# Performance work log

Measured on AMD Instinct MI355X. Metric: run time of the kernel, lower is better.

## Reference

```python
import jax, jax.numpy as jnp
import numpy as np

N_HEAD = 16
W = 128  # one-sided window = attention_window // 2


def setup_inputs() -> dict:
    key = jax.random.key(0)
    ks = jax.random.split(key, 6)
    B, S, D = 4, 1536, 1024
    init = lambda k: jax.random.normal(k, (D, D), jnp.float32) * 0.02
    return {
        "x": jax.random.normal(ks[0], (B, S, D), jnp.float32),
        "Wq": init(ks[1]), "bq": jnp.zeros((D,), jnp.float32),
        "Wk": init(ks[2]),
        "Wv": init(ks[3]), "bv": jnp.zeros((D,), jnp.float32),
        "Wo": init(ks[4]), "bo": jnp.zeros((D,), jnp.float32),
    }


def _local_attention(q, k, v, w):
    """Sliding-window attention. q,k,v: [B,H,S,Dh]; q,k pre-scaled.
    Returns context [B,H,S,Dh] and banded logits qk [B,S,H,2w+1] (fp32)."""
    B, H, S, Dh = q.shape
    C = S // w  # number of w-sized query chunks
    pad = [(0, 0), (0, 0), (w, w), (0, 0)]
    kp = jnp.pad(k, pad)
    vp = jnp.pad(v, pad)
    # key/value chunks: chunk c sees padded positions [c*w, c*w + 3w)
    idx = jnp.arange(C)[:, None] * w + jnp.arange(3 * w)[None, :]  # [C,3w]
    kc = kp[:, :, idx]                      # [B,H,C,3w,Dh]
    vc = vp[:, :, idx]                      # [B,H,C,3w,Dh]
    qc = q.reshape(B, H, C, w, Dh)          # [B,H,C,w,Dh]
    scores = jnp.einsum('bhcxd,bhcyd->bhcxy', qc, kc)  # [B,H,C,w,3w]
    # extract diagonal band: query x attends to chunk-local keys y = x .. x+2w
    xi = jnp.arange(w)[:, None]             # [w,1]
    jj = jnp.arange(2 * w + 1)[None, :]     # [1,2w+1]
    y = xi + jj                             # [w,2w+1], values in [0,3w)
    band = jnp.take_along_axis(scores, y[None, None, None], axis=-1)  # [B,H,C,w,2w+1]
    # mask positions whose absolute key index falls outside [0,S)
    key_pos = jnp.arange(C)[:, None, None] * w + xi[None] + jj[None] - w  # [C,w,2w+1]
    valid = (key_pos >= 0) & (key_pos < S)
    band = jnp.where(valid[None, None], band, -jnp.inf)
    prob = jax.nn.softmax(band.astype(jnp.float32), axis=-1).astype(q.dtype)
    # scatter band probs back to chunk layout, then contract with value chunks
    scat = jnp.zeros_like(scores).at[..., xi, y].set(prob)  # [B,H,C,w,3w]
    ctx = jnp.einsum('bhcxy,bhcyd->bhcxd', scat, vc).reshape(B, H, S, Dh)
    qk = band.astype(jnp.float32).reshape(B, H, S, 2 * w + 1).transpose(0, 2, 1, 3)
    return ctx, qk


def reference(x, Wq, bq, Wk, Wv, bv, Wo, bo):
    B, S, D = x.shape
    H, Dh = N_HEAD, D // N_HEAD
    scale = Dh ** (-0.25)
    q = ((x @ Wq.T + bq).reshape(B, S, H, Dh).transpose(0, 2, 1, 3)) * scale
    k = ((x @ Wk.T).reshape(B, S, H, Dh).transpose(0, 2, 1, 3)) * scale
    v = (x @ Wv.T + bv).reshape(B, S, H, Dh).transpose(0, 2, 1, 3)
    ctx, qk = _local_attention(q, k, v, W)
    wv = ctx.transpose(0, 2, 1, 3).reshape(B, S, D)
    out = wv @ Wo.T + bo
    return out, qk
```

## Files before the change

kernel.cpp:

```cpp
#include <hip/hip_runtime.h>

#define S_LEN  1536
#define NH     16
#define DHEAD  64
#define WIN    128
#define BAND   257
#define DMODEL 1024
#define BATCH  4
#define MROWS  (BATCH * S_LEN)

#define SQ    32
#define SWIN  (SQ + 2*WIN)
#define WKEYS 320
#define PST   296

#define NEG_BIG (-3.0e38f)

typedef __attribute__((ext_vector_type(8))) short frag_ab;
typedef __attribute__((ext_vector_type(4))) float frag_cd;
typedef __attribute__((ext_vector_type(8))) unsigned short ushort8v;

__device__ __forceinline__ unsigned short f2bf(float f) {
  unsigned u = __float_as_uint(f);
  u += 0x7FFFu + ((u >> 16) & 1u);
  return (unsigned short)(u >> 16);
}
__device__ __forceinline__ float bf2f(unsigned short h) {
  return __uint_as_float(((unsigned)h) << 16);
}

__device__ __forceinline__ void gload16(const unsigned short* g, unsigned short* l) {
  __builtin_amdgcn_global_load_lds(
      (const __attribute__((address_space(1))) unsigned int*)g,
      (__attribute__((address_space(3))) unsigned int*)l, 16, 0, 0);
}

__global__ __launch_bounds__(256)
void convert_hilo(const float* __restrict__ src, unsigned short* __restrict__ hi,
                  unsigned short* __restrict__ lo, int n4)
{
  const int i = blockIdx.x * 256 + threadIdx.x;
  if (i >= n4) return;
  const float4 v = reinterpret_cast<const float4*>(src)[i];
  unsigned short h0 = f2bf(v.x), h1 = f2bf(v.y), h2 = f2bf(v.z), h3 = f2bf(v.w);
  unsigned short l0 = f2bf(v.x - bf2f(h0)), l1 = f2bf(v.y - bf2f(h1));
  unsigned short l2 = f2bf(v.z - bf2f(h2)), l3 = f2bf(v.w - bf2f(h3));
  uint2 hp, lp;
  hp.x = (unsigned)h0 | ((unsigned)h1 << 16); hp.y = (unsigned)h2 | ((unsigned)h3 << 16);
  lp.x = (unsigned)l0 | ((unsigned)l1 << 16); lp.y = (unsigned)l2 | ((unsigned)l3 << 16);
  reinterpret_cast<uint2*>(hi)[i] = hp;
  reinterpret_cast<uint2*>(lo)[i] = lp;
}

__global__ __launch_bounds__(256)
void copy_f4(const float4* __restrict__ src, float4* __restrict__ dst, int n4)
{
  const int i = blockIdx.x * 256 + threadIdx.x;
  if (i < n4) dst[i] = src[i];
}

__global__ __launch_bounds__(256)
void mfma_gemm_bt(const unsigned short* __restrict__ Ah_g,
                  const unsigned short* __restrict__ Al_g,
                  const unsigned short* __restrict__ Bh_g,
                  const unsigned short* __restrict__ Bl_g,
                  const float* __restrict__ bias, float scale,
                  float* __restrict__ Cf,
                  unsigned short* __restrict__ Ch,
                  unsigned short* __restrict__ Cl, int mode)
{
  __shared__ __align__(16) unsigned short Ah[128*32];
  __shared__ __align__(16) unsigned short Al[128*32];
  __shared__ __align__(16) unsigned short Bh[64*32];
  __shared__ __align__(16) unsigned short Bl[64*32];

  const int t    = threadIdx.x;
  const int wave = t >> 6, lane = t & 63;
  const int wr   = wave >> 1, wc = wave & 1;
  const int m0   = blockIdx.y * 128;
  const int n0   = blockIdx.x * 64;

  frag_cd acc[4][2];
#pragma unroll
  for (int i = 0; i < 4; ++i)
#pragma unroll
    for (int j = 0; j < 2; ++j) acc[i][j] = (frag_cd){0.f,0.f,0.f,0.f};

  const int srow = lane >> 2;
  const int scol = (lane & 3) * 8;
  const unsigned short* pa0 = Ah_g + (size_t)(m0 + wave*32      + srow) * DMODEL + scol;
  const unsigned short* pa1 = Ah_g + (size_t)(m0 + wave*32 + 16 + srow) * DMODEL + scol;
  const unsigned short* qa0 = Al_g + (size_t)(m0 + wave*32      + srow) * DMODEL + scol;
  const unsigned short* qa1 = Al_g + (size_t)(m0 + wave*32 + 16 + srow) * DMODEL + scol;
  const unsigned short* pb  = Bh_g + (size_t)(n0 + wave*16      + srow) * DMODEL + scol;
  const unsigned short* qb  = Bl_g + (size_t)(n0 + wave*16      + srow) * DMODEL + scol;
  unsigned short* lA0 = &Ah[(wave*32)*32];
  unsigned short* lA1 = &Ah[(wave*32+16)*32];
  unsigned short* lL0 = &Al[(wave*32)*32];
  unsigned short* lL1 = &Al[(wave*32+16)*32];
  unsigned short* lB  = &Bh[(wave*16)*32];
  unsigned short* lBl = &Bl[(wave*16)*32];

  const int l16  = lane & 15;
  const int koff = (lane >> 4) * 8;
  int ofsA[4], ofsB[2];
#pragma unroll
  for (int i = 0; i < 4; ++i) ofsA[i] = (wr*64 + i*16 + l16)*32 + koff;
#pragma unroll
  for (int j = 0; j < 2; ++j) ofsB[j] = (wc*32 + j*16 + l16)*32 + koff;

  for (int k0 = 0; k0 < DMODEL; k0 += 32) {
    gload16(pa0, lA0); gload16(pa1, lA1);
    gload16(qa0, lL0); gload16(qa1, lL1);
    gload16(pb,  lB);  gload16(qb,  lBl);
    pa0 += 32; pa1 += 32; qa0 += 32; qa1 += 32; pb += 32; qb += 32;
    __syncthreads();

    frag_ab ah[4], alr[4], bh[2], blr[2];
#pragma unroll
    for (int i = 0; i < 4; ++i) {
      ah[i]  = *reinterpret_cast<const frag_ab*>(&Ah[ofsA[i]]);
      alr[i] = *reinterpret_cast<const frag_ab*>(&Al[ofsA[i]]);
    }
#pragma unroll
    for (int j = 0; j < 2; ++j) {
      bh[j]  = *reinterpret_cast<const frag_ab*>(&Bh[ofsB[j]]);
      blr[j] = *reinterpret_cast<const frag_ab*>(&Bl[ofsB[j]]);
    }
#pragma unroll
    for (int i = 0; i < 4; ++i)
#pragma unroll
      for (int j = 0; j < 2; ++j) {
        acc[i][j] = __builtin_amdgcn_mfma_f32_16x16x32_bf16(ah[i],  bh[j],  acc[i][j], 0,0,0);
        acc[i][j] = __builtin_amdgcn_mfma_f32_16x16x32_bf16(ah[i],  blr[j], acc[i][j], 0,0,0);
        acc[i][j] = __builtin_amdgcn_mfma_f32_16x16x32_bf16(alr[i], bh[j],  acc[i][j], 0,0,0);
      }
    __syncthreads();
  }

  const int rg = lane >> 4;
#pragma unroll
  for (int j = 0; j < 2; ++j) {
    const int n = n0 + wc*32 + j*16 + l16;
    const float bval = bias ? bias[n] : 0.f;
#pragma unroll
    for (int i = 0; i < 4; ++i) {
#pragma unroll
      for (int r = 0; r < 4; ++r) {
        const int m = m0 + wr*64 + i*16 + rg*4 + r;
        const float v = (acc[i][j][r] + bval) * scale;
        if (mode) {
          const int b = m / S_LEN;
          const int s = m - b * S_LEN;
          const int hh = n >> 6, dh = n & 63;
          const size_t idx = ((size_t)((b*NH + hh)*S_LEN + s))*DHEAD + dh;
          const unsigned short hv = f2bf(v);
          Ch[idx] = hv;
          Cl[idx] = f2bf(v - bf2f(hv));
        } else {
          Cf[(size_t)m * DMODEL + n] = v;
        }
      }
    }
  }
}

__global__ __launch_bounds__(256)
void attn_fused(const unsigned short* __restrict__ Qh_g, const unsigned short* __restrict__ Ql_g,
                const unsigned short* __restrict__ Kh_g, const unsigned short* __restrict__ Kl_g,
                const unsigned short* __restrict__ Vh_g, const unsigned short* __restrict__ Vl_g,
                float* __restrict__ qk,
                unsigned short* __restrict__ ctx_hi, unsigned short* __restrict__ ctx_lo)
{
  __shared__ __align__(16) unsigned char arena[59904];
  unsigned short* Khs = (unsigned short*)(arena);
  unsigned short* Kls = (unsigned short*)(arena + 20480);
  unsigned short* Qhs = (unsigned short*)(arena + 40960);
  unsigned short* Qls = (unsigned short*)(arena + 43008);
  unsigned short* Pth = (unsigned short*)(arena);
  unsigned short* Ptl = (unsigned short*)(arena + 18944);
  float*          red = (float*)(arena + 37888);
  unsigned short* Vth = (unsigned short*)(arena + 40960);
  unsigned short* Vtl = (unsigned short*)(arena + 50432);

  const int t    = threadIdx.x;
  const int wave = t >> 6, lane = t & 63;

  const int lid  = blockIdx.x;
  const int xcd  = lid & 7;
  const int idx  = lid >> 3;
  const int qblk = xcd*6 + (idx % 6);
  const int hb   = idx / 6;
  const int h    = hb & 15, b = hb >> 4;
  const int qa0  = qblk * SQ;
  const int ws0  = qa0 - WIN;

  const size_t ho = (size_t)(b*NH + h) * S_LEN * DHEAD;
  const unsigned short* Qh = Qh_g + ho;
  const unsigned short* Ql = Ql_g + ho;
  const unsigned short* Kh = Kh_g + ho;
  const unsigned short* Kl = Kl_g + ho;
  const unsigned short* Vh = Vh_g + ho;
  const unsigned short* Vl = Vl_g + ho;

  const int l16  = lane & 15;
  const int grp  = lane >> 4;
  const int koff = grp * 8;
  const int srow = lane >> 2;
  const int scol = (lane & 3) * 8;

  frag_cd acc[2][5];
#pragma unroll
  for (int tm = 0; tm < 2; ++tm)
#pragma unroll
    for (int tn = 0; tn < 5; ++tn) acc[tm][tn] = (frag_cd){0.f,0.f,0.f,0.f};

  for (int p = 0; p < 2; ++p) {
    const int d0 = p * 32;
    if (p) __syncthreads();
#pragma unroll
    for (int i = 0; i < 5; ++i) {
      const int r0 = wave*80 + i*16;
      const ptrdiff_t g = (ptrdiff_t)(ws0 + r0 + srow) * DHEAD + d0 + scol;
      gload16(Kh + g, &Khs[r0*32]);
      gload16(Kl + g, &Kls[r0*32]);
    }
    if (wave < 2) {
      const unsigned short* src = wave ? Ql : Qh;
      unsigned short* dst = wave ? Qls : Qhs;
#pragma unroll
      for (int i = 0; i < 2; ++i) {
        const ptrdiff_t g = (ptrdiff_t)(qa0 + i*16 + srow) * DHEAD + d0 + scol;
        gload16(src + g, &dst[i*16*32]);
      }
    }
    __syncthreads();

    frag_ab ah[2], al[2];
#pragma unroll
    for (int tm = 0; tm < 2; ++tm) {
      const int o = (tm*16 + l16)*32 + koff;
      ah[tm] = *reinterpret_cast<const frag_ab*>(&Qhs[o]);
      al[tm] = *reinterpret_cast<const frag_ab*>(&Qls[o]);
    }
#pragma unroll
    for (int tn = 0; tn < 5; ++tn) {
      const int o = (wave*80 + tn*16 + l16)*32 + koff;
      frag_ab bh = *reinterpret_cast<const frag_ab*>(&Khs[o]);
      frag_ab bl = *reinterpret_cast<const frag_ab*>(&Kls[o]);
#pragma unroll
      for (int tm = 0; tm < 2; ++tm) {
        acc[tm][tn] = __builtin_amdgcn_mfma_f32_16x16x32_bf16(ah[tm], bh, acc[tm][tn], 0,0,0);
        acc[tm][tn] = __builtin_amdgcn_mfma_f32_16x16x32_bf16(ah[tm], bl, acc[tm][tn], 0,0,0);
        acc[tm][tn] = __builtin_amdgcn_mfma_f32_16x16x32_bf16(al[tm], bh, acc[tm][tn], 0,0,0);
      }
    }
  }

#pragma unroll
  for (int tm = 0; tm < 2; ++tm)
#pragma unroll
    for (int tn = 0; tn < 5; ++tn)
#pragma unroll
      for (int r = 0; r < 4; ++r) {
        const int x  = tm*16 + grp*4 + r;
        const int yw = wave*80 + tn*16 + l16;
        const int j  = yw - x;
        const int kp = ws0 + yw;
        const bool ok = (j >= 0) & (j < BAND) & (kp >= 0) & (kp < S_LEN);
        acc[tm][tn][r] = ok ? acc[tm][tn][r] : NEG_BIG;
      }
#pragma unroll
  for (int tm = 0; tm < 2; ++tm)
#pragma unroll
    for (int r = 0; r < 4; ++r) {
      const int x = tm*16 + grp*4 + r;
      float* qrow = qk + ((size_t)(b*S_LEN + qa0 + x)*NH + h) * BAND;
#pragma unroll
      for (int tn = 0; tn < 5; ++tn) {
        const int yw = wave*80 + tn*16 + l16;
        const int j  = yw - x;
        if (j >= 0 && j < BAND) qrow[j] = acc[tm][tn][r];
      }
    }

  __syncthreads();

  ushort8v vreg[5];
  const unsigned short* vsrc = (wave & 2) ? Vl : Vh;
  unsigned short*       vdst = (wave & 2) ? Vtl : Vth;
  const int dsub = (wave & 1) * 8;

  auto loadV = [&](int c) {
    const int d0 = c*16 + dsub;
#pragma unroll
    for (int it = 0; it < 5; ++it) {
      const int y = it*64 + lane;
      ushort8v v = {0,0,0,0,0,0,0,0};
      if (y < SWIN) {
        const int kp = ws0 + y;
        if (kp >= 0 && kp < S_LEN)
          v = *reinterpret_cast<const ushort8v*>(vsrc + (size_t)kp*DHEAD + d0);
      }
      vreg[it] = v;
    }
  };
  auto writeV = [&]() {
#pragma unroll
    for (int it = 0; it < 5; ++it) {
      const int y = it*64 + lane;
      if (y < SWIN) {
#pragma unroll
        for (int e = 0; e < 8; ++e) vdst[(dsub+e)*PST + y] = vreg[it][e];
      }
    }
  };

  loadV(0);
  float gm[2][4];
#pragma unroll
  for (int tm = 0; tm < 2; ++tm)
#pragma unroll
    for (int r = 0; r < 4; ++r) {
      float m = acc[tm][0][r];
#pragma unroll
      for (int tn = 1; tn < 5; ++tn) m = fmaxf(m, acc[tm][tn][r]);
      m = fmaxf(m, __shfl_xor(m, 1, 64));
      m = fmaxf(m, __shfl_xor(m, 2, 64));
      m = fmaxf(m, __shfl_xor(m, 4, 64));
      m = fmaxf(m, __shfl_xor(m, 8, 64));
      gm[tm][r] = m;
      if (l16 == 0) red[(0*4 + wave)*32 + tm*16 + grp*4 + r] = m;
    }
  {
    const uint4 z = make_uint4(0u,0u,0u,0u);
    uint4* pz = reinterpret_cast<uint4*>(arena);
    for (int i = t; i < 37888/16; i += 256) pz[i] = z;
  }
  writeV();
  loadV(1);
  __syncthreads();

#pragma unroll
  for (int tm = 0; tm < 2; ++tm)
#pragma unroll
    for (int r = 0; r < 4; ++r) {
      const int x = tm*16 + grp*4 + r;
      float m = red[0*128 + 0*32 + x];
      m = fmaxf(m, red[0*128 + 1*32 + x]);
      m = fmaxf(m, red[0*128 + 2*32 + x]);
      m = fmaxf(m, red[0*128 + 3*32 + x]);
      gm[tm][r] = m;
      float s = 0.f;
#pragma unroll
      for (int tn = 0; tn < 5; ++tn) {
        const float e = __expf(acc[tm][tn][r] - m);
        acc[tm][tn][r] = e;
        s += e;
      }
      s += __shfl_xor(s, 1, 64);
      s += __shfl_xor(s, 2, 64);
      s += __shfl_xor(s, 4, 64);
      s += __shfl_xor(s, 8, 64);
      if (l16 == 0) red[(1*4 + wave)*32 + x] = s;
    }
  __syncthreads();

#pragma unroll
  for (int tm = 0; tm < 2; ++tm)
#pragma unroll
    for (int r = 0; r < 4; ++r) {
      const int x = tm*16 + grp*4 + r;
      const float gs = red[128 + 0*32 + x] + red[128 + 1*32 + x]
                     + red[128 + 2*32 + x] + red[128 + 3*32 + x];
      const float inv = 1.f / gs;
#pragma unroll
      for (int tn = 0; tn < 5; ++tn) {
        const int yw = wave*80 + tn*16 + l16;
        const int j  = yw - x;
        if (yw < SWIN && j >= 0 && j < BAND) {
          const float p = acc[tm][tn][r] * inv;
          const unsigned short ph = f2bf(p);
          Pth[x*PST + yw] = ph;
          Ptl[x*PST + yw] = f2bf(p - bf2f(ph));
        }
      }
    }
  __syncthreads();

  for (int c = 0; c < 4; ++c) {
    if ((wave & 1) == 0) {
      const int wr = wave >> 1;
      frag_cd a = (frag_cd){0.f,0.f,0.f,0.f};
#pragma unroll
      for (int ks = 0; ks < SWIN/32; ++ks) {
        const int kk = ks*32 + koff;
        frag_ab ph = *reinterpret_cast<const frag_ab*>(&Pth[(wr*16 + l16)*PST + kk]);
        frag_ab pl = *reinterpret_cast<const frag_ab*>(&Ptl[(wr*16 + l16)*PST + kk]);
        frag_ab vh = *reinterpret_cast<const frag_ab*>(&Vth[l16*PST + kk]);
        frag_ab vl = *reinterpret_cast<const frag_ab*>(&Vtl[l16*PST + kk]);
        a = __builtin_amdgcn_mfma_f32_16x16x32_bf16(ph, vh, a, 0,0,0);
        a = __builtin_amdgcn_mfma_f32_16x16x32_bf16(ph, vl, a, 0,0,0);
        a = __builtin_amdgcn_mfma_f32_16x16x32_bf16(pl, vh, a, 0,0,0);
      }
      const int d = c*16 + l16;
#pragma unroll
      for (int r = 0; r < 4; ++r) {
        const int x = wr*16 + grp*4 + r;
        const size_t oidx = ((size_t)(b*S_LEN + qa0 + x))*DMODEL + h*DHEAD + d;
        const float v = a[r];
        const unsigned short hv = f2bf(v);
        ctx_hi[oidx] = hv;
        ctx_lo[oidx] = f2bf(v - bf2f(hv));
      }
    }
    __syncthreads();
    if (c < 3) {
      writeV();
      if (c < 2) loadV(c + 2);
      __syncthreads();
    }
  }
}

extern "C" void kernel_launch(void* const* d_in, const int* in_sizes, int n_in,
                              void* d_out, int out_size, void* d_ws, size_t ws_size,
                              hipStream_t stream) {
  const float* x  = (const float*)d_in[0];
  const float* Wq = (const float*)d_in[1];
  const float* bq = (const float*)d_in[2];
  const float* Wk = (const float*)d_in[3];
  const float* Wv = (const float*)d_in[4];
  const float* bv = (const float*)d_in[5];
  const float* Wo = (const float*)d_in[6];
  const float* bo = (const float*)d_in[7];

  float* out = (float*)d_out;
  float* qk  = out + (size_t)MROWS * DMODEL;

  const size_t NX = (size_t)MROWS * DMODEL;
  const size_t NW = (size_t)DMODEL * DMODEL;

  unsigned short* xh  = (unsigned short*)qk;
  unsigned short* xl  = xh  + NX;
  unsigned short* wqh = xl  + NX;
  unsigned short* wql = wqh + NW;
  unsigned short* wkh = wql + NW;
  unsigned short* wkl = wkh + NW;
  unsigned short* wvh = wkl + NW;
  unsigned short* wvl = wvh + NW;

  unsigned short* Qh = (unsigned short*)d_ws;
  unsigned short* Ql = Qh + NX;
  unsigned short* Kh = Ql + NX;
  unsigned short* Kl = Kh + NX;
  unsigned short* Vh = Kl + NX;
  unsigned short* Vl = Vh + NX;

  unsigned short* ctxh = (unsigned short*)out;
  unsigned short* ctxl = ctxh + NX;
  unsigned short* woh  = Kh;
  unsigned short* wol  = Kh + NW;
  float* outTmp = (float*)d_ws;

  const float scale = 0.35355339059327373f;

  dim3 blk(256);
  hipLaunchKernelGGL(convert_hilo, dim3(NX/1024), blk, 0, stream, x,  xh,  xl,  (int)(NX/4));
  hipLaunchKernelGGL(convert_hilo, dim3(NW/1024), blk, 0, stream, Wq, wqh, wql, (int)(NW/4));
  hipLaunchKernelGGL(convert_hilo, dim3(NW/1024), blk, 0, stream, Wk, wkh, wkl, (int)(NW/4));
  hipLaunchKernelGGL(convert_hilo, dim3(NW/1024), blk, 0, stream, Wv, wvh, wvl, (int)(NW/4));

  dim3 gg(DMODEL/64, MROWS/128);
  hipLaunchKernelGGL(mfma_gemm_bt, gg, blk, 0, stream, xh, xl, wqh, wql, bq,      scale,
                     (float*)nullptr, Qh, Ql, 1);
  hipLaunchKernelGGL(mfma_gemm_bt, gg, blk, 0, stream, xh, xl, wkh, wkl, nullptr, scale,
                     (float*)nullptr, Kh, Kl, 1);
  hipLaunchKernelGGL(mfma_gemm_bt, gg, blk, 0, stream, xh, xl, wvh, wvl, bv,      1.0f,
                     (float*)nullptr, Vh, Vl, 1);

  hipLaunchKernelGGL(attn_fused, dim3((S_LEN/SQ)*NH*BATCH), blk, 0, stream,
                     Qh, Ql, Kh, Kl, Vh, Vl, qk, ctxh, ctxl);

  hipLaunchKernelGGL(convert_hilo, dim3(NW/1024), blk, 0, stream, Wo, woh, wol, (int)(NW/4));

  hipLaunchKernelGGL(mfma_gemm_bt, gg, blk, 0, stream, ctxh, ctxl, woh, wol, bo, 1.0f,
                     outTmp, (unsigned short*)nullptr, (unsigned short*)nullptr, 0);
  hipLaunchKernelGGL(copy_f4, dim3(NX/1024), blk, 0, stream,
                     (const float4*)outTmp, (float4*)out, (int)(NX/4));
}
```

Measured before the change: 509.7 us.

## Split PV stage into producer/consumer waves and shrink LDS for higher occupancy

The P·V stage is reorganised so each 16-wide B tile packs the high and low halves of V for eight head dims. This needs two MFMAs per k-step instead of three, and a lane shuffle folds the two halves back together. Waves 2-3 become V loaders with RA/RB register double-buffering, while waves 0-1 do the MFMAs with the P-high fragments held in registers across chunks. The single V buffer cuts shared memory and the launch bounds now request 3 blocks per CU, aiming for more concurrency. In exchange, half the waves sit out the matrix work, the stage runs eight synchronised chunks instead of four, and the extra P-low×V-low product is harmless but wasted work.

```diff
diff --git a/kernel.cpp b/kernel.cpp
--- a/kernel.cpp
+++ b/kernel.cpp
@@ -165,14 +165,14 @@
   }
 }
 
-__global__ __launch_bounds__(256)
+__global__ __launch_bounds__(256, 3)
 void attn_fused(const unsigned short* __restrict__ Qh_g, const unsigned short* __restrict__ Ql_g,
                 const unsigned short* __restrict__ Kh_g, const unsigned short* __restrict__ Kl_g,
                 const unsigned short* __restrict__ Vh_g, const unsigned short* __restrict__ Vl_g,
                 float* __restrict__ qk,
                 unsigned short* __restrict__ ctx_hi, unsigned short* __restrict__ ctx_lo)
 {
-  __shared__ __align__(16) unsigned char arena[59904];
+  __shared__ __align__(16) unsigned char arena[48384];
   unsigned short* Khs = (unsigned short*)(arena);
   unsigned short* Kls = (unsigned short*)(arena + 20480);
   unsigned short* Qhs = (unsigned short*)(arena + 40960);
@@ -180,8 +180,7 @@
   unsigned short* Pth = (unsigned short*)(arena);
   unsigned short* Ptl = (unsigned short*)(arena + 18944);
   float*          red = (float*)(arena + 37888);
-  unsigned short* Vth = (unsigned short*)(arena + 40960);
-  unsigned short* Vtl = (unsigned short*)(arena + 50432);
+  unsigned short* Vs  = (unsigned short*)(arena + 38912);
 
   const int t    = threadIdx.x;
   const int wave = t >> 6, lane = t & 63;
@@ -286,13 +285,12 @@
 
   __syncthreads();
 
-  ushort8v vreg[5];
-  const unsigned short* vsrc = (wave & 2) ? Vl : Vh;
-  unsigned short*       vdst = (wave & 2) ? Vtl : Vth;
-  const int dsub = (wave & 1) * 8;
-
-  auto loadV = [&](int c) {
-    const int d0 = c*16 + dsub;
+  const unsigned short* vsrc = (wave == 3) ? Vl : Vh;
+  const int vrow0 = (wave == 3) ? 8 : 0;
+  ushort8v RA[5], RB[5];
+
+  auto loadVto = [&](int c, ushort8v* R) {
+    const int d0 = c*8;
 #pragma unroll
     for (int it = 0; it < 5; ++it) {
       const int y = it*64 + lane;
@@ -302,22 +300,21 @@
         if (kp >= 0 && kp < S_LEN)
           v = *reinterpret_cast<const ushort8v*>(vsrc + (size_t)kp*DHEAD + d0);
       }
-      vreg[it] = v;
+      R[it] = v;
     }
   };
-  auto writeV = [&]() {
+  auto writeVfrom = [&](ushort8v* R) {
 #pragma unroll
     for (int it = 0; it < 5; ++it) {
       const int y = it*64 + lane;
       if (y < SWIN) {
 #pragma unroll
-        for (int e = 0; e < 8; ++e) vdst[(dsub+e)*PST + y] = vreg[it][e];
+        for (int e = 0; e < 8; ++e) Vs[(vrow0 + e)*PST + y] = R[it][e];
       }
     }
   };
 
-  loadV(0);
-  float gm[2][4];
+  if (wave >= 2) loadVto(0, RA);
 #pragma unroll
   for (int tm = 0; tm < 2; ++tm)
 #pragma unroll
@@ -329,7 +326,6 @@
       m = fmaxf(m, __shfl_xor(m, 2, 64));
       m = fmaxf(m, __shfl_xor(m, 4, 64));
       m = fmaxf(m, __shfl_xor(m, 8, 64));
-      gm[tm][r] = m;
       if (l16 == 0) red[(0*4 + wave)*32 + tm*16 + grp*4 + r] = m;
     }
   {
@@ -337,10 +333,10 @@
     uint4* pz = reinterpret_cast<uint4*>(arena);
     for (int i = t; i < 37888/16; i += 256) pz[i] = z;
   }
-  writeV();
-  loadV(1);
+  if (wave >= 2) writeVfrom(RA);
   __syncthreads();
 
+  if (wave >= 2) loadVto(1, RA);
 #pragma unroll
   for (int tm = 0; tm < 2; ++tm)
 #pragma unroll
@@ -350,7 +346,6 @@
       m = fmaxf(m, red[0*128 + 1*32 + x]);
       m = fmaxf(m, red[0*128 + 2*32 + x]);
       m = fmaxf(m, red[0*128 + 3*32 + x]);
-      gm[tm][r] = m;
       float s = 0.f;
 #pragma unroll
       for (int tn = 0; tn < 5; ++tn) {
@@ -388,38 +383,48 @@
     }
   __syncthreads();
 
-  for (int c = 0; c < 4; ++c) {
-    if ((wave & 1) == 0) {
-      const int wr = wave >> 1;
-      frag_cd a = (frag_cd){0.f,0.f,0.f,0.f};
-#pragma unroll
-      for (int ks = 0; ks < SWIN/32; ++ks) {
+  frag_ab phf[9];
+  if (wave < 2) {
+#pragma unroll
+    for (int ks = 0; ks < 9; ++ks)
+      phf[ks] = *reinterpret_cast<const frag_ab*>(&Pth[(wave*16 + l16)*PST + ks*32 + koff]);
+  }
+
+#pragma unroll
+  for (int c = 0; c < 8; ++c) {
+    frag_cd pacc = (frag_cd){0.f,0.f,0.f,0.f};
+    if (wave < 2) {
+#pragma unroll
+      for (int ks = 0; ks < 9; ++ks) {
         const int kk = ks*32 + koff;
-        frag_ab ph = *reinterpret_cast<const frag_ab*>(&Pth[(wr*16 + l16)*PST + kk]);
-        frag_ab pl = *reinterpret_cast<const frag_ab*>(&Ptl[(wr*16 + l16)*PST + kk]);
-        frag_ab vh = *reinterpret_cast<const frag_ab*>(&Vth[l16*PST + kk]);
-        frag_ab vl = *reinterpret_cast<const frag_ab*>(&Vtl[l16*PST + kk]);
-        a = __builtin_amdgcn_mfma_f32_16x16x32_bf16(ph, vh, a, 0,0,0);
-        a = __builtin_amdgcn_mfma_f32_16x16x32_bf16(ph, vl, a, 0,0,0);
-        a = __builtin_amdgcn_mfma_f32_16x16x32_bf16(pl, vh, a, 0,0,0);
-      }
-      const int d = c*16 + l16;
-#pragma unroll
-      for (int r = 0; r < 4; ++r) {
-        const int x = wr*16 + grp*4 + r;
-        const size_t oidx = ((size_t)(b*S_LEN + qa0 + x))*DMODEL + h*DHEAD + d;
-        const float v = a[r];
-        const unsigned short hv = f2bf(v);
-        ctx_hi[oidx] = hv;
-        ctx_lo[oidx] = f2bf(v - bf2f(hv));
-      }
+        frag_ab pl = *reinterpret_cast<const frag_ab*>(&Ptl[(wave*16 + l16)*PST + kk]);
+        frag_ab vb = *reinterpret_cast<const frag_ab*>(&Vs[l16*PST + kk]);
+        pacc = __builtin_amdgcn_mfma_f32_16x16x32_bf16(phf[ks], vb, pacc, 0,0,0);
+        pacc = __builtin_amdgcn_mfma_f32_16x16x32_bf16(pl,      vb, pacc, 0,0,0);
+      }
+    } else {
+      if (c < 6) loadVto(c + 2, (c & 1) ? RA : RB);
     }
     __syncthreads();
-    if (c < 3) {
-      writeV();
-      if (c < 2) loadV(c + 2);
-      __syncthreads();
-    }
+    if (wave < 2) {
+#pragma unroll
+      for (int r = 0; r < 4; ++r) pacc[r] += __shfl_xor(pacc[r], 8, 64);
+      if (l16 < 8) {
+        const int d = c*8 + l16;
+#pragma unroll
+        for (int r = 0; r < 4; ++r) {
+          const int x = wave*16 + grp*4 + r;
+          const size_t oidx = ((size_t)(b*S_LEN + qa0 + x))*DMODEL + h*DHEAD + d;
+          const float v = pacc[r];
+          const unsigned short hv = f2bf(v);
+          ctx_hi[oidx] = hv;
+          ctx_lo[oidx] = f2bf(v - bf2f(hv));
+        }
+      }
+    } else {
+      if (c < 7) writeVfrom((c & 1) ? RB : RA);
+    }
+    if (c < 7) __syncthreads();
   }
 }
 
```

Result: faster. 492.2 us (-3.4%).
